# Optimization experiments

Measured on AMD Instinct MI355X. Metric: run time of the kernel, lower is better.

## Reference

```python
import jax, jax.numpy as jnp
import numpy as np

# BiDAF-style co-attention with memory_len=2. Dropout is inference-mode identity.

def setup_inputs() -> dict:
    key = jax.random.key(0)
    k1, k2, k3, k4, k5 = jax.random.split(key, 5)
    d = 1024
    inp = jax.random.normal(k1, (8, 4096, d), dtype=jnp.float32)
    mem = jax.random.normal(k2, (8, 2, d), dtype=jnp.float32)
    w_input = jax.random.normal(k3, (d,), dtype=jnp.float32) * (1.0 / np.sqrt(d))
    w_memory = jax.random.normal(k4, (d,), dtype=jnp.float32) * (1.0 / np.sqrt(d))
    dot_scale = jax.random.uniform(k5, (d,), dtype=jnp.float32, minval=0.0, maxval=1.0 / np.sqrt(d))
    return {"input": inp, "memory": mem, "w_input": w_input, "w_memory": w_memory, "dot_scale": dot_scale}


def reference(input, memory, w_input, w_memory, dot_scale):
    # input: [b, L, d]; memory: [b, M=2, d]
    input_dot = jnp.einsum('bld,d->bl', input, w_input)[..., None]        # [b, L, 1]
    memory_dot = jnp.einsum('bmd,d->bm', memory, w_memory)[:, None, :]    # [b, 1, M]
    cross_dot = jnp.einsum('bld,bmd->blm', input * dot_scale, memory)     # [b, L, M]
    att = input_dot + memory_dot + cross_dot                              # [b, L, M]
    weight_one = jax.nn.softmax(att, axis=-1)                             # [b, L, M]
    output_one = jnp.einsum('blm,bmd->bld', weight_one, memory)           # [b, L, d]
    weight_two = jax.nn.softmax(jnp.max(att, axis=-1), axis=-1)           # [b, L]
    output_two = jnp.einsum('bl,bld->bd', weight_two, input)[:, None, :]  # [b, 1, d]
    return jnp.concatenate([input, output_one, input * output_one, output_two * output_one], axis=-1)
```

## Files before the change

kernel.cpp:

```cpp
#include <hip/hip_runtime.h>
#include <stdint.h>


#define BB 8
#define LL 4096
#define DD 1024
#define NBLK 1024
#define BPB 128
#define RPB 32
#define RPW 8

typedef float f32x4 __attribute__((ext_vector_type(4)));

static __device__ __forceinline__ f32x4 nt_load4(const float* p) {
    return __builtin_nontemporal_load((const f32x4*)p);
}
static __device__ __forceinline__ void nt_store4(float* p, f32x4 v) {
    __builtin_nontemporal_store(v, (f32x4*)p);
}
static __device__ __forceinline__ float hsum4(f32x4 v) {
    return (v.x + v.y) + (v.z + v.w);
}

__global__ __launch_bounds__(256) void kA(const float* __restrict__ input,
                                          const float* __restrict__ memory,
                                          const float* __restrict__ w_in,
                                          const float* __restrict__ w_mem,
                                          const float* __restrict__ ds,
                                          float* __restrict__ w0buf,
                                          float* __restrict__ pmax,
                                          float* __restrict__ pz,
                                          float* __restrict__ pacc,
                                          float* __restrict__ out) {
    int blk = blockIdx.x;
    int b = blk >> 7, chunk = blk & 127;
    int t = threadIdx.x;
    int wave = t >> 6, lane = t & 63;

    f32x4 rc0[4], rc1[4], rm0[4], rm1[4], acc[4];
    float md0 = 0.f, md1 = 0.f;
    {
        const float* m0p = memory + (size_t)b * 2 * DD;
        const float* m1p = m0p + DD;
#pragma unroll
        for (int k = 0; k < 4; ++k) {
            int i = 4 * (lane + 64 * k);
            f32x4 m0 = *(const f32x4*)(m0p + i);
            f32x4 m1 = *(const f32x4*)(m1p + i);
            f32x4 wi = *(const f32x4*)(w_in + i);
            f32x4 dv = *(const f32x4*)(ds + i);
            f32x4 wm = *(const f32x4*)(w_mem + i);
            rm0[k] = m0; rm1[k] = m1;
            rc0[k] = wi + dv * m0;
            rc1[k] = wi + dv * m1;
            md0 += hsum4(m0 * wm);
            md1 += hsum4(m1 * wm);
            acc[k] = (f32x4)(0.f);
        }
        for (int off = 32; off; off >>= 1) {
            md0 += __shfl_xor(md0, off);
            md1 += __shfl_xor(md1, off);
        }
    }

    float lmax = -1e30f, zsum = 0.f;
    int l0 = chunk * RPB + wave * RPW;
    const float* inb = input + (size_t)b * LL * DD;
    for (int r = 0; r < RPW; ++r) {
        int l = l0 + r;
        const float* row = inb + (size_t)l * DD;
        f32x4 x[4];
#pragma unroll
        for (int k = 0; k < 4; ++k) x[k] = nt_load4(row + 4 * (lane + 64 * k));

        f32x4 s0 = x[0] * rc0[0], s1 = x[0] * rc1[0];
#pragma unroll
        for (int k = 1; k < 4; ++k) { s0 += x[k] * rc0[k]; s1 += x[k] * rc1[k]; }
        float a0 = hsum4(s0), a1 = hsum4(s1);
        for (int off = 32; off; off >>= 1) {
            a0 += __shfl_xor(a0, off);
            a1 += __shfl_xor(a1, off);
        }
        a0 += md0; a1 += md1;

        float w0 = 1.f / (1.f + __expf(a1 - a0));
        float w1 = 1.f - w0;
        if (lane == 0) w0buf[(size_t)b * LL + l] = w0;
        float ml = fmaxf(a0, a1);

        float e;
        if (ml > lmax) {
            float s = __expf(lmax - ml);
            zsum *= s;
#pragma unroll
            for (int k = 0; k < 4; ++k) acc[k] *= s;
            lmax = ml;
            e = 1.f;
        } else {
            e = __expf(ml - lmax);
        }
        zsum += e;

        float* orow = out + (size_t)(b * LL + l) * (4 * DD);
#pragma unroll
        for (int k = 0; k < 4; ++k) {
            int i = 4 * (lane + 64 * k);
            f32x4 o1 = w0 * rm0[k] + w1 * rm1[k];
            nt_store4(orow + i, x[k]);
            nt_store4(orow + DD + i, o1);
            nt_store4(orow + 2 * DD + i, x[k] * o1);
            acc[k] += e * x[k];
        }
    }

    __shared__ float swm[4], swz[4];
    __shared__ __align__(16) float swacc[4][DD];
    if (lane == 0) { swm[wave] = lmax; swz[wave] = zsum; }
    __syncthreads();
    float bmax = fmaxf(fmaxf(swm[0], swm[1]), fmaxf(swm[2], swm[3]));
    float f = __expf(lmax - bmax);
#pragma unroll
    for (int k = 0; k < 4; ++k) {
        *(f32x4*)(swacc[wave] + 4 * (lane + 64 * k)) = f * acc[k];
    }
    __syncthreads();
    {
        f32x4 s = *(const f32x4*)(swacc[0] + 4 * t) + *(const f32x4*)(swacc[1] + 4 * t)
                + *(const f32x4*)(swacc[2] + 4 * t) + *(const f32x4*)(swacc[3] + 4 * t);
        *(f32x4*)(pacc + (size_t)blk * DD + 4 * t) = s;
        if (t == 0) {
            float bz = 0.f;
#pragma unroll
            for (int w = 0; w < 4; ++w) bz += swz[w] * __expf(swm[w] - bmax);
            pmax[blk] = bmax;
            pz[blk]   = bz;
        }
    }
}

__global__ __launch_bounds__(256) void kB(const float* __restrict__ pmax,
                                          const float* __restrict__ pz,
                                          const float* __restrict__ pacc,
                                          float* __restrict__ out2) {
    int b = blockIdx.x, t = threadIdx.x;
    __shared__ float se[BPB];
    const float* pm  = pmax + b * BPB;
    const float* pzb = pz   + b * BPB;
    float m = -1e30f;
    for (int i = 0; i < BPB; ++i) m = fmaxf(m, pm[i]);
    if (t < BPB) se[t] = __expf(pm[t] - m);
    __syncthreads();
    float Z = 0.f;
    for (int i = 0; i < BPB; ++i) Z = fmaf(pzb[i], se[i], Z);
    float invZ = 1.f / Z;

    const float* P = pacc + (size_t)b * BPB * DD;
    f32x4 a = (f32x4)(0.f);
    for (int i = 0; i < BPB; ++i) {
        a += se[i] * *(const f32x4*)(P + (size_t)i * DD + 4 * t);
    }
    a *= invZ;
    *(f32x4*)(out2 + (size_t)b * DD + 4 * t) = a;
}

__global__ __launch_bounds__(256) void kE(const float* __restrict__ memory,
                                          const float* __restrict__ w0buf,
                                          const float* __restrict__ out2,
                                          float* __restrict__ out) {
    int blk = blockIdx.x;
    int b = blk >> 8, chunk = blk & 255;
    int t = threadIdx.x;
    f32x4 m0 = *(const f32x4*)(memory + (size_t)b * 2 * DD + 4 * t);
    f32x4 m1 = *(const f32x4*)(memory + (size_t)b * 2 * DD + DD + 4 * t);
    f32x4 o2 = *(const f32x4*)(out2 + (size_t)b * DD + 4 * t);
    const float* w0b = w0buf + (size_t)b * LL + chunk * 16;
    for (int r = 0; r < 16; ++r) {
        float w0 = w0b[r];
        float w1 = 1.f - w0;
        f32x4 o1 = w0 * m0 + w1 * m1;
        float* orow = out + (size_t)(b * LL + chunk * 16 + r) * (4 * DD) + 3 * DD;
        nt_store4(orow + 4 * t, o2 * o1);
    }
}

extern "C" void kernel_launch(void* const* d_in, const int* in_sizes, int n_in,
                              void* d_out, int out_size, void* d_ws, size_t ws_size,
                              hipStream_t stream) {
    const float* input  = (const float*)d_in[0];
    const float* memory = (const float*)d_in[1];
    const float* w_in   = (const float*)d_in[2];
    const float* w_mem  = (const float*)d_in[3];
    const float* ds     = (const float*)d_in[4];
    float* out = (float*)d_out;

    float* ws    = (float*)d_ws;
    float* w0buf = ws;
    float* pmax  = ws + 32768;
    float* pz    = ws + 33792;
    float* out2  = ws + 34816;
    float* pacc  = ws + 43008;

    kA<<<NBLK, 256, 0, stream>>>(input, memory, w_in, w_mem, ds,
                                 w0buf, pmax, pz, pacc, out);
    kB<<<BB,   256, 0, stream>>>(pmax, pz, pacc, out2);
    kE<<<2048, 256, 0, stream>>>(memory, w0buf, out2, out);
}
```

Before: 664.3 us.

## Double block counts across kernels and split reduction across more blocks

Halves rows per block in the main pass so twice as many blocks run, and regroups the output stores so each of the three output segments is written in its own loop. Splits the cross-block reduction kernel four ways along the feature dimension, using scalar loads, to get more parallelism. Doubles the number of blocks in the final write kernel. This doubles the partial-accumulator workspace that kA writes and kB reads back, adding reduction traffic in exchange for better occupancy and latency hiding.

```diff
diff --git a/kernel.cpp b/kernel.cpp
--- a/kernel.cpp
+++ b/kernel.cpp
@@ -5,10 +5,10 @@
 #define BB 8
 #define LL 4096
 #define DD 1024
-#define NBLK 1024
-#define BPB 128
-#define RPB 32
-#define RPW 8
+#define NBLK 2048
+#define BPB 256
+#define RPB 16
+#define RPW 4
 
 typedef float f32x4 __attribute__((ext_vector_type(4)));
 
@@ -33,7 +33,7 @@
                                           float* __restrict__ pacc,
                                           float* __restrict__ out) {
     int blk = blockIdx.x;
-    int b = blk >> 7, chunk = blk & 127;
+    int b = blk >> 8, chunk = blk & 255;
     int t = threadIdx.x;
     int wave = t >> 6, lane = t & 63;
 
@@ -102,15 +102,20 @@
         zsum += e;
 
         float* orow = out + (size_t)(b * LL + l) * (4 * DD);
-#pragma unroll
-        for (int k = 0; k < 4; ++k) {
-            int i = 4 * (lane + 64 * k);
-            f32x4 o1 = w0 * rm0[k] + w1 * rm1[k];
-            nt_store4(orow + i, x[k]);
-            nt_store4(orow + DD + i, o1);
-            nt_store4(orow + 2 * DD + i, x[k] * o1);
-            acc[k] += e * x[k];
-        }
+        f32x4 o1v[4];
+#pragma unroll
+        for (int k = 0; k < 4; ++k) o1v[k] = w0 * rm0[k] + w1 * rm1[k];
+#pragma unroll
+        for (int k = 0; k < 4; ++k)
+            nt_store4(orow + 4 * (lane + 64 * k), x[k]);
+#pragma unroll
+        for (int k = 0; k < 4; ++k)
+            nt_store4(orow + DD + 4 * (lane + 64 * k), o1v[k]);
+#pragma unroll
+        for (int k = 0; k < 4; ++k)
+            nt_store4(orow + 2 * DD + 4 * (lane + 64 * k), x[k] * o1v[k]);
+#pragma unroll
+        for (int k = 0; k < 4; ++k) acc[k] += e * x[k];
     }
 
     __shared__ float swm[4], swz[4];
@@ -142,43 +147,43 @@
                                           const float* __restrict__ pz,
                                           const float* __restrict__ pacc,
                                           float* __restrict__ out2) {
-    int b = blockIdx.x, t = threadIdx.x;
+    int bid = blockIdx.x;
+    int b = bid >> 2, q = bid & 3;
+    int t = threadIdx.x;
+    int d = q * 256 + t;
     __shared__ float se[BPB];
     const float* pm  = pmax + b * BPB;
     const float* pzb = pz   + b * BPB;
     float m = -1e30f;
     for (int i = 0; i < BPB; ++i) m = fmaxf(m, pm[i]);
-    if (t < BPB) se[t] = __expf(pm[t] - m);
+    se[t] = __expf(pm[t] - m);
     __syncthreads();
     float Z = 0.f;
     for (int i = 0; i < BPB; ++i) Z = fmaf(pzb[i], se[i], Z);
     float invZ = 1.f / Z;
 
-    const float* P = pacc + (size_t)b * BPB * DD;
-    f32x4 a = (f32x4)(0.f);
-    for (int i = 0; i < BPB; ++i) {
-        a += se[i] * *(const f32x4*)(P + (size_t)i * DD + 4 * t);
-    }
-    a *= invZ;
-    *(f32x4*)(out2 + (size_t)b * DD + 4 * t) = a;
+    const float* P = pacc + (size_t)b * BPB * DD + d;
+    float a = 0.f;
+    for (int i = 0; i < BPB; ++i) a = fmaf(se[i], P[(size_t)i * DD], a);
+    out2[(size_t)b * DD + d] = a * invZ;
 }
 
 __global__ __launch_bounds__(256) void kE(const float* __restrict__ memory,
                                           const float* __restrict__ w0buf,
                                           const float* __restrict__ out2,
                                           float* __restrict__ out) {
-    int blk = blockIdx.x;
-    int b = blk >> 8, chunk = blk & 255;
+    int bid = blockIdx.x;
+    int b = bid >> 9, chunk = bid & 511;
     int t = threadIdx.x;
     f32x4 m0 = *(const f32x4*)(memory + (size_t)b * 2 * DD + 4 * t);
     f32x4 m1 = *(const f32x4*)(memory + (size_t)b * 2 * DD + DD + 4 * t);
     f32x4 o2 = *(const f32x4*)(out2 + (size_t)b * DD + 4 * t);
-    const float* w0b = w0buf + (size_t)b * LL + chunk * 16;
-    for (int r = 0; r < 16; ++r) {
+    const float* w0b = w0buf + (size_t)b * LL + chunk * 8;
+    for (int r = 0; r < 8; ++r) {
         float w0 = w0b[r];
         float w1 = 1.f - w0;
         f32x4 o1 = w0 * m0 + w1 * m1;
-        float* orow = out + (size_t)(b * LL + chunk * 16 + r) * (4 * DD) + 3 * DD;
+        float* orow = out + (size_t)(b * LL + chunk * 8 + r) * (4 * DD) + 3 * DD;
         nt_store4(orow + 4 * t, o2 * o1);
     }
 }
@@ -196,12 +201,12 @@
     float* ws    = (float*)d_ws;
     float* w0buf = ws;
     float* pmax  = ws + 32768;
-    float* pz    = ws + 33792;
-    float* out2  = ws + 34816;
-    float* pacc  = ws + 43008;
+    float* pz    = ws + 34816;
+    float* out2  = ws + 36864;
+    float* pacc  = ws + 45056;
 
     kA<<<NBLK, 256, 0, stream>>>(input, memory, w_in, w_mem, ds,
                                  w0buf, pmax, pz, pacc, out);
-    kB<<<BB,   256, 0, stream>>>(pmax, pz, pacc, out2);
-    kE<<<2048, 256, 0, stream>>>(memory, w0buf, out2, out);
-}
+    kB<<<32,   256, 0, stream>>>(pmax, pz, pacc, out2);
+    kE<<<4096, 256, 0, stream>>>(memory, w0buf, out2, out);
+}
```

Measured after the change: 646.7 us. 1.03x faster.
